# Kernel tuning notes

Measured on AMD Instinct MI355X. Metric: run time of the kernel, lower is better.

## Reference

```python
import jax, jax.numpy as jnp
import numpy as np

GAMMA = 3.0
ALPHA = 1.5
GRID = 32
EPS = 1e-7

N_BOXES = 4_000_000


def _ciou(box1, box2, eps=EPS):
    """Ultralytics bbox_iou with xywh=True, CIoU=True. Returns shape (N,)."""
    x1, y1, w1, h1 = box1[..., 0], box1[..., 1], box1[..., 2], box1[..., 3]
    x2, y2, w2, h2 = box2[..., 0], box2[..., 1], box2[..., 2], box2[..., 3]
    # xywh -> xyxy
    b1x1, b1x2 = x1 - w1 * 0.5, x1 + w1 * 0.5
    b1y1, b1y2 = y1 - h1 * 0.5, y1 + h1 * 0.5
    b2x1, b2x2 = x2 - w2 * 0.5, x2 + w2 * 0.5
    b2y1, b2y2 = y2 - h2 * 0.5, y2 + h2 * 0.5
    # intersection
    iw = jnp.clip(jnp.minimum(b1x2, b2x2) - jnp.maximum(b1x1, b2x1), 0.0, None)
    ih = jnp.clip(jnp.minimum(b1y2, b2y2) - jnp.maximum(b1y1, b2y1), 0.0, None)
    inter = iw * ih
    union = w1 * h1 + w2 * h2 - inter + eps
    iou = inter / union
    # enclosing box diagonal and center distance
    cw = jnp.maximum(b1x2, b2x2) - jnp.minimum(b1x1, b2x1)
    ch = jnp.maximum(b1y2, b2y2) - jnp.minimum(b1y1, b2y1)
    c2 = cw * cw + ch * ch + eps
    rho2 = ((b2x1 + b2x2 - b1x1 - b1x2) ** 2 + (b2y1 + b2y2 - b1y1 - b1y2) ** 2) * 0.25
    # aspect-ratio term; alpha is computed under no_grad in torch -> stop_gradient
    v = (4.0 / (jnp.pi ** 2)) * (jnp.arctan(w2 / h2) - jnp.arctan(w1 / h1)) ** 2
    a = jax.lax.stop_gradient(v / (v - iou + (1.0 + eps)))
    return iou - (rho2 / c2 + v * a)


def _density_map(boxes, grid_size=GRID):
    # scatter-add histogram over box centers (equivalent of the Python for-loop)
    gx = jnp.clip((boxes[..., 0] * grid_size).astype(jnp.int32), 0, grid_size - 1)
    gy = jnp.clip((boxes[..., 1] * grid_size).astype(jnp.int32), 0, grid_size - 1)
    density = jnp.zeros((grid_size, grid_size), boxes.dtype).at[gy, gx].add(1.0)
    return density / jnp.max(density)


def setup_inputs() -> dict:
    key = jax.random.key(0)
    k1, k2 = jax.random.split(key)
    pred_boxes = jax.random.uniform(k1, (N_BOXES, 4), dtype=jnp.float32)
    target_boxes = jax.random.uniform(k2, (N_BOXES, 4), dtype=jnp.float32)
    return {"pred_boxes": pred_boxes, "target_boxes": target_boxes}


def reference(pred_boxes, target_boxes):
    iou = _ciou(pred_boxes, target_boxes)                      # (N,)
    target_areas = target_boxes[..., 2] * target_boxes[..., 3]
    scale_weight = 1.0 / (target_areas + 1e-7)                 # (N,)
    base = (1.0 - iou) ** GAMMA * scale_weight                 # (N,)
    density = _density_map(target_boxes)                       # (32,32)
    density_weight = 1.0 + ALPHA * density                     # (32,32)
    # original: mean over the (1,32,32,N) outer-product broadcast, which
    # factorizes exactly as mean(base) * mean(density_weight)
    return jnp.mean(base) * jnp.mean(density_weight)
```

## Files before the change

### kernel.cpp

```cpp
#include <hip/hip_runtime.h>
#include <math.h>


#define NBLK 1024
#define BLOCK 512
#define GRID_BINS 1024

__device__ __forceinline__ float rcpf(float x) { return __builtin_amdgcn_rcpf(x); }

__device__ __forceinline__ float fast_atan(float x) {
    float ax = fabsf(x);
    bool big = ax > 1.0f;
    float t = big ? rcpf(ax) : ax;
    float s = t * t;
    float p = -0.0117212f;
    p = __builtin_fmaf(p, s, 0.05265332f);
    p = __builtin_fmaf(p, s, -0.11643287f);
    p = __builtin_fmaf(p, s, 0.19354346f);
    p = __builtin_fmaf(p, s, -0.33262347f);
    p = __builtin_fmaf(p, s, 0.99997726f);
    float r = t * p;
    r = big ? 1.57079632679f - r : r;
    return copysignf(r, x);
}

__device__ __forceinline__ float ciou_base(float4 p, float4 t, unsigned* lhist, bool valid) {
    float x1 = p.x, y1 = p.y, w1 = p.z, h1 = p.w;
    float x2 = t.x, y2 = t.y, w2 = t.z, h2 = t.w;
    float b1x1 = x1 - w1 * 0.5f, b1x2 = x1 + w1 * 0.5f;
    float b1y1 = y1 - h1 * 0.5f, b1y2 = y1 + h1 * 0.5f;
    float b2x1 = x2 - w2 * 0.5f, b2x2 = x2 + w2 * 0.5f;
    float b2y1 = y2 - h2 * 0.5f, b2y2 = y2 + h2 * 0.5f;
    float iw = fmaxf(fminf(b1x2, b2x2) - fmaxf(b1x1, b2x1), 0.0f);
    float ih = fmaxf(fminf(b1y2, b2y2) - fmaxf(b1y1, b2y1), 0.0f);
    float inter = iw * ih;
    float uni = w1 * h1 + w2 * h2 - inter + 1e-7f;
    float iou = inter * rcpf(uni);
    float cw = fmaxf(b1x2, b2x2) - fminf(b1x1, b2x1);
    float ch = fmaxf(b1y2, b2y2) - fminf(b1y1, b2y1);
    float c2 = cw * cw + ch * ch + 1e-7f;
    float ddx = b2x1 + b2x2 - b1x1 - b1x2;
    float ddy = b2y1 + b2y2 - b1y1 - b1y2;
    float rho2 = (ddx * ddx + ddy * ddy) * 0.25f;
    float dv = fast_atan((w2 * h1 - w1 * h2) * rcpf(h1 * h2 + w1 * w2));
    float v = 0.4052847345693511f * (dv * dv);
    float a = v * rcpf(v - iou + (1.0f + 1e-7f));
    float ciou = iou - (rho2 * rcpf(c2) + v * a);
    float om = 1.0f - ciou;
    int gx = min(max((int)(x2 * 32.0f), 0), 31);
    int gy = min(max((int)(y2 * 32.0f), 0), 31);
    if (valid) atomicAdd(&lhist[gy * 32 + gx], 1u);
    float base = om * om * om * rcpf(w2 * h2 + 1e-7f);
    return valid ? base : 0.0f;
}

__global__ __launch_bounds__(BLOCK) void dosa_main(
    const float4* __restrict__ pred, const float4* __restrict__ tgt, int n,
    unsigned short* __restrict__ partHist, double* __restrict__ partSum)
{
    __shared__ unsigned lhist[GRID_BINS];
    __shared__ double wsum[BLOCK / 64];
    for (int i = threadIdx.x; i < GRID_BINS; i += BLOCK) lhist[i] = 0u;
    __syncthreads();

    const int T = NBLK * BLOCK;
    const int i0 = blockIdx.x * BLOCK + threadIdx.x;
    float fsum = 0.0f;

    float4 p0 = pred[i0 + 0 * T], q0 = tgt[i0 + 0 * T];
    float4 p1 = pred[i0 + 1 * T], q1 = tgt[i0 + 1 * T];
    float4 p2 = pred[i0 + 2 * T], q2 = tgt[i0 + 2 * T];
    float4 p3 = pred[i0 + 3 * T], q3 = tgt[i0 + 3 * T];
    __builtin_amdgcn_sched_barrier(0);
    fsum += ciou_base(p0, q0, lhist, true);
    fsum += ciou_base(p1, q1, lhist, true);
    fsum += ciou_base(p2, q2, lhist, true);
    fsum += ciou_base(p3, q3, lhist, true);

    const bool v7 = (i0 + 7 * T) < n;
    const int i7 = v7 ? (i0 + 7 * T) : i0;
    float4 p4 = pred[i0 + 4 * T], q4 = tgt[i0 + 4 * T];
    float4 p5 = pred[i0 + 5 * T], q5 = tgt[i0 + 5 * T];
    float4 p6 = pred[i0 + 6 * T], q6 = tgt[i0 + 6 * T];
    float4 p7 = pred[i7],         q7 = tgt[i7];
    __builtin_amdgcn_sched_barrier(0);
    fsum += ciou_base(p4, q4, lhist, true);
    fsum += ciou_base(p5, q5, lhist, true);
    fsum += ciou_base(p6, q6, lhist, true);
    fsum += ciou_base(p7, q7, lhist, v7);

    for (int off = 32; off > 0; off >>= 1)
        fsum += __shfl_down(fsum, off, 64);
    int lane = threadIdx.x & 63;
    int wid = threadIdx.x >> 6;
    if (lane == 0) wsum[wid] = (double)fsum;
    __syncthreads();
    for (int b = threadIdx.x; b < GRID_BINS; b += BLOCK)
        partHist[(size_t)blockIdx.x * GRID_BINS + b] = (unsigned short)lhist[b];
    if (threadIdx.x == 0) {
        double s = 0.0;
        for (int w = 0; w < BLOCK / 64; ++w) s += wsum[w];
        partSum[blockIdx.x] = s;
    }
}

__global__ __launch_bounds__(1024) void dosa_hist_max(
    const unsigned short* __restrict__ partHist, unsigned* __restrict__ blockMax)
{
    __shared__ unsigned red[1024];
    const int b0 = blockIdx.x * 16;
    const int binOff = threadIdx.x & 15;
    const int rowgrp = threadIdx.x >> 4;
    unsigned s = 0;
#pragma unroll
    for (int k = 0; k < NBLK / 64; ++k)
        s += partHist[(size_t)(rowgrp + k * 64) * GRID_BINS + b0 + binOff];
    red[threadIdx.x] = s;
    __syncthreads();
    for (int off = 512; off >= 16; off >>= 1) {
        if (threadIdx.x < off) red[threadIdx.x] += red[threadIdx.x + off];
        __syncthreads();
    }
    if (threadIdx.x == 0) {
        unsigned m = 0;
        for (int j = 0; j < 16; ++j) m = max(m, red[j]);
        blockMax[blockIdx.x] = m;
    }
}

__global__ __launch_bounds__(1024) void dosa_final(
    const unsigned* __restrict__ blockMax, const double* __restrict__ partSum,
    float* __restrict__ out, int n)
{
    __shared__ unsigned sm[1024];
    __shared__ double sd[1024];
    int t = threadIdx.x;
    sm[t] = (t < 64) ? blockMax[t] : 0u;
    sd[t] = partSum[t];
    __syncthreads();
    for (int off = 512; off > 0; off >>= 1) {
        if (t < off) {
            sm[t] = max(sm[t], sm[t + off]);
            sd[t] += sd[t + off];
        }
        __syncthreads();
    }
    if (t == 0) {
        double meanBase = sd[0] / (double)n;
        double meanW = 1.0 + 1.5 * ((double)n / (double)sm[0]) / 1024.0;
        out[0] = (float)(meanBase * meanW);
    }
}

extern "C" void kernel_launch(void* const* d_in, const int* in_sizes, int n_in,
                              void* d_out, int out_size, void* d_ws, size_t ws_size,
                              hipStream_t stream) {
    const float4* pred = (const float4*)d_in[0];
    const float4* tgt  = (const float4*)d_in[1];
    int n = in_sizes[0] / 4;

    unsigned short* partHist = (unsigned short*)d_ws;
    double* partSum = (double*)((char*)d_ws + (size_t)NBLK * GRID_BINS * 2);
    unsigned* blockMax = (unsigned*)((char*)partSum + NBLK * sizeof(double));
    float* out = (float*)d_out;

    dosa_main<<<NBLK, BLOCK, 0, stream>>>(pred, tgt, n, partHist, partSum);
    dosa_hist_max<<<64, 1024, 0, stream>>>(partHist, blockMax);
    dosa_final<<<1, 1024, 0, stream>>>(blockMax, partSum, out, n);
}
```

Before: 35.10 us.

## Merge histogram-max and final reduction into one kernel with last-block finish

Replaces the two trailing kernels (64-block histogram max, then a single-block final) with one reduce kernel of 1025 blocks. Each block sums one bin across partial histograms, or sums the partial base sums, then folds its result in with atomicMax or a plain store. A ticket counter picks the last block to finish, and that block writes the output. This removes one kernel launch and its serialization in exchange for more, smaller blocks doing strided uncoalesced reads and using global atomics.

Result: slower. 109.9 us (+213.2%).

```diff
diff --git a/kernel.cpp b/kernel.cpp
--- a/kernel.cpp
+++ b/kernel.cpp
@@ -56,11 +56,13 @@
 
 __global__ __launch_bounds__(BLOCK) void dosa_main(
     const float4* __restrict__ pred, const float4* __restrict__ tgt, int n,
-    unsigned short* __restrict__ partHist, double* __restrict__ partSum)
+    unsigned short* __restrict__ partHist, double* __restrict__ partSum,
+    unsigned* __restrict__ ctrl )
 {
     __shared__ unsigned lhist[GRID_BINS];
     __shared__ double wsum[BLOCK / 64];
     for (int i = threadIdx.x; i < GRID_BINS; i += BLOCK) lhist[i] = 0u;
+    if (blockIdx.x == 0 && threadIdx.x < 2) ctrl[threadIdx.x] = 0u;
     __syncthreads();
 
     const int T = NBLK * BLOCK;
@@ -104,51 +106,51 @@
     }
 }
 
-__global__ __launch_bounds__(1024) void dosa_hist_max(
-    const unsigned short* __restrict__ partHist, unsigned* __restrict__ blockMax)
-{
-    __shared__ unsigned red[1024];
-    const int b0 = blockIdx.x * 16;
-    const int binOff = threadIdx.x & 15;
-    const int rowgrp = threadIdx.x >> 4;
-    unsigned s = 0;
-#pragma unroll
-    for (int k = 0; k < NBLK / 64; ++k)
-        s += partHist[(size_t)(rowgrp + k * 64) * GRID_BINS + b0 + binOff];
-    red[threadIdx.x] = s;
-    __syncthreads();
-    for (int off = 512; off >= 16; off >>= 1) {
-        if (threadIdx.x < off) red[threadIdx.x] += red[threadIdx.x + off];
-        __syncthreads();
-    }
-    if (threadIdx.x == 0) {
-        unsigned m = 0;
-        for (int j = 0; j < 16; ++j) m = max(m, red[j]);
-        blockMax[blockIdx.x] = m;
-    }
-}
-
-__global__ __launch_bounds__(1024) void dosa_final(
-    const unsigned* __restrict__ blockMax, const double* __restrict__ partSum,
+__global__ __launch_bounds__(256) void dosa_reduce(
+    const unsigned short* __restrict__ partHist, const double* __restrict__ partSum,
+    unsigned* __restrict__ ctrl, double* __restrict__ baseSum,
     float* __restrict__ out, int n)
 {
-    __shared__ unsigned sm[1024];
-    __shared__ double sd[1024];
-    int t = threadIdx.x;
-    sm[t] = (t < 64) ? blockMax[t] : 0u;
-    sd[t] = partSum[t];
+    __shared__ unsigned ru[256];
+    __shared__ double rd[256];
+    const int t = threadIdx.x;
+
+    if (blockIdx.x < GRID_BINS) {
+        const int bin = blockIdx.x;
+        unsigned s = 0;
+#pragma unroll
+        for (int k = 0; k < NBLK / 256; ++k)
+            s += partHist[(size_t)(t + k * 256) * GRID_BINS + bin];
+        ru[t] = s;
+        __syncthreads();
+        for (int off = 128; off > 0; off >>= 1) {
+            if (t < off) ru[t] += ru[t + off];
+            __syncthreads();
+        }
+        if (t == 0) atomicMax(&ctrl[0], ru[0]);
+    } else {
+        double s = 0.0;
+#pragma unroll
+        for (int k = 0; k < NBLK / 256; ++k)
+            s += partSum[t + k * 256];
+        rd[t] = s;
+        __syncthreads();
+        for (int off = 128; off > 0; off >>= 1) {
+            if (t < off) rd[t] += rd[t + off];
+            __syncthreads();
+        }
+        if (t == 0) *baseSum = rd[0];
+    }
+
+    __threadfence();
     __syncthreads();
-    for (int off = 512; off > 0; off >>= 1) {
-        if (t < off) {
-            sm[t] = max(sm[t], sm[t + off]);
-            sd[t] += sd[t + off];
+    if (t == 0) {
+        unsigned old = atomicAdd(&ctrl[1], 1u);
+        if (old == GRID_BINS) {
+            double meanBase = *baseSum / (double)n;
+            double meanW = 1.0 + 1.5 * ((double)n / (double)ctrl[0]) / 1024.0;
+            out[0] = (float)(meanBase * meanW);
         }
-        __syncthreads();
-    }
-    if (t == 0) {
-        double meanBase = sd[0] / (double)n;
-        double meanW = 1.0 + 1.5 * ((double)n / (double)sm[0]) / 1024.0;
-        out[0] = (float)(meanBase * meanW);
     }
 }
 
@@ -161,10 +163,10 @@
 
     unsigned short* partHist = (unsigned short*)d_ws;
     double* partSum = (double*)((char*)d_ws + (size_t)NBLK * GRID_BINS * 2);
-    unsigned* blockMax = (unsigned*)((char*)partSum + NBLK * sizeof(double));
+    unsigned* ctrl = (unsigned*)((char*)partSum + NBLK * sizeof(double));
+    double* baseSum = (double*)((char*)ctrl + 16);
     float* out = (float*)d_out;
 
-    dosa_main<<<NBLK, BLOCK, 0, stream>>>(pred, tgt, n, partHist, partSum);
-    dosa_hist_max<<<64, 1024, 0, stream>>>(partHist, blockMax);
-    dosa_final<<<1, 1024, 0, stream>>>(blockMax, partSum, out, n);
+    dosa_main<<<NBLK, BLOCK, 0, stream>>>(pred, tgt, n, partHist, partSum, ctrl);
+    dosa_reduce<<<GRID_BINS + 1, 256, 0, stream>>>(partHist, partSum, ctrl, baseSum, out, n);
 }
```
